# Optimization experiments

Measured on AMD Instinct MI355X. Metric: run time of the kernel, lower is better.

Reference implementation:

```python
import jax, jax.numpy as jnp
import numpy as np

SEQ, B, H, OUT = 128, 256, 1024, 128


def _linear_params(key, out_dim, in_dim):
    kw, kb = jax.random.split(key)
    bound = 1.0 / np.sqrt(in_dim)
    W = jax.random.uniform(kw, (out_dim, in_dim), jnp.float32, -bound, bound)
    b = jax.random.uniform(kb, (out_dim,), jnp.float32, -bound, bound)
    return W, b


def setup_inputs() -> dict:
    key = jax.random.key(0)
    keys = jax.random.split(key, 10)
    x = jax.random.normal(keys[0], (SEQ, B), jnp.float32)
    Wfx, bfx = _linear_params(keys[1], H, 1)
    Wfh, bfh = _linear_params(keys[2], H, H)
    Wix, bix = _linear_params(keys[3], H, 1)
    Wih, bih = _linear_params(keys[4], H, H)
    Wgx, bgx = _linear_params(keys[5], H, 1)
    Wgh, bgh = _linear_params(keys[6], H, H)
    Wox, box = _linear_params(keys[7], H, 1)
    Woh, boh = _linear_params(keys[8], H, H)
    Wph, bph = _linear_params(keys[9], OUT, H)
    return dict(x=x, Wfx=Wfx, bfx=bfx, Wfh=Wfh, bfh=bfh,
                Wix=Wix, bix=bix, Wih=Wih, bih=bih,
                Wgx=Wgx, bgx=bgx, Wgh=Wgh, bgh=bgh,
                Wox=Wox, box=box, Woh=Woh, boh=boh,
                Wph=Wph, bph=bph)


def reference(x, Wfx, bfx, Wfh, bfh, Wix, bix, Wih, bih,
              Wgx, bgx, Wgh, bgh, Wox, box, Woh, boh, Wph, bph):
    # Fuse the 8 per-gate linears into two GEMMs per step (x-proj and h-proj),
    # gate order: f, i, g, o.
    Wx = jnp.concatenate([Wfx, Wix, Wgx, Wox], axis=0)      # (4H, 1)
    bx = jnp.concatenate([bfx, bix, bgx, box], axis=0)       # (4H,)
    Wh = jnp.concatenate([Wfh, Wih, Wgh, Woh], axis=0)       # (4H, H)
    bh = jnp.concatenate([bfh, bih, bgh, boh], axis=0)       # (4H,)
    Hdim = Wfh.shape[0]
    Bsz = x.shape[1]

    # x projection has input_dim=1: precompute for all timesteps at once.
    zx_all = x[:, :, None] * Wx[:, 0][None, None, :] + bx     # (S, B, 4H)

    def step(carry, zx):
        h, c = carry
        z = zx + h @ Wh.T + bh                                # (B, 4H)
        f = jax.nn.sigmoid(z[:, 0 * Hdim:1 * Hdim])
        i = jax.nn.sigmoid(z[:, 1 * Hdim:2 * Hdim])
        g = jnp.tanh(z[:, 2 * Hdim:3 * Hdim])
        o = jax.nn.sigmoid(z[:, 3 * Hdim:4 * Hdim])
        c = g * i + c * f
        h = jnp.tanh(c) * o
        return (h, c), None

    h0 = jnp.zeros((Bsz, Hdim), x.dtype)
    c0 = jnp.zeros((Bsz, Hdim), x.dtype)
    (h, c), _ = jax.lax.scan(step, (h0, c0), zx_all)
    logits = h @ Wph.T + bph                                  # (B, OUT)
    return jax.nn.softmax(logits, axis=-1)
```

## Files before the change

kernel.cpp:

```cpp
#include <hip/hip_runtime.h>
#include <hip/hip_fp16.h>
#include <cstdint>
#include <cstddef>

#define SEQ   128
#define BATCH 256
#define HDIM  1024
#define ODIM  128
#define NBLK  256

typedef _Float16 half_t;
typedef _Float16 half8 __attribute__((ext_vector_type(8)));
typedef float    f32x4 __attribute__((ext_vector_type(4)));
typedef unsigned long long u64;

#define LDS_P_OFF    131072
#define LDS_HS_OFF   (LDS_P_OFF + 2 * 64 * 36 * 4)
#define LDS_BYTES    (LDS_HS_OFF + 64 * 16 * 2)

#define HBUF_BYTES   524288
#define FLAGS_OFF    ((size_t)129 * HBUF_BYTES)

__device__ __forceinline__ float sigmoidf_(float z) {
    return 1.0f / (1.0f + __expf(-z));
}
__device__ __forceinline__ float tanhf_(float z) {
    z = fminf(fmaxf(z, -30.0f), 30.0f);
    float e = __expf(2.0f * z);
    return (e - 1.0f) / (e + 1.0f);
}

__global__ __launch_bounds__(256) void lstm_init(int* __restrict__ flags) {
    flags[blockIdx.x * 256 + threadIdx.x] = 0;
}

__global__ __launch_bounds__(512, 2) void lstm_persist(
    const float* __restrict__ x,
    const float* __restrict__ Wfh, const float* __restrict__ Wih,
    const float* __restrict__ Wgh, const float* __restrict__ Woh,
    const float* __restrict__ Wfx, const float* __restrict__ Wix,
    const float* __restrict__ Wgx, const float* __restrict__ Wox,
    const float* __restrict__ bfx, const float* __restrict__ bix,
    const float* __restrict__ bgx, const float* __restrict__ box,
    const float* __restrict__ bfh, const float* __restrict__ bih,
    const float* __restrict__ bgh, const float* __restrict__ boh,
    const float* __restrict__ Wph, const float* __restrict__ bph,
    char* __restrict__ wsbase, float* __restrict__ out)
{
    extern __shared__ char smem[];
    half_t* Bs = (half_t*)smem;
    float*  P  = (float*)(smem + LDS_P_OFF);
    half_t* Hs = (half_t*)(smem + LDS_HS_OFF);
    int* flags = (int*)(wsbase + FLAGS_OFF);

    const int tid  = threadIdx.x;
    const int blk  = blockIdx.x;
    const int grp  = blk & 3;
    const int by   = blk >> 2;
    const int m0   = grp << 6;
    const int u0   = by << 4;

    const int w    = tid >> 6;
    const int lane = tid & 63;
    const int l15  = lane & 15;
    const int q    = lane >> 4;
    const int kh   = w >> 2;
    const int mh   = w & 3;

    {
        const float* Wh[4] = {Wfh, Wih, Wgh, Woh};
        for (int d = tid; d < 8192; d += 512) {
            const int ul = d & 15, qq = (d >> 4) & 3, g = (d >> 6) & 3;
            const int kk = (d >> 8) & 15, kh2 = d >> 12;
            const float* src = Wh[g] + (size_t)(u0 + ul) * HDIM
                             + kh2 * 512 + kk * 32 + qq * 8;
            const float4 v0 = *(const float4*)src;
            const float4 v1 = *(const float4*)(src + 4);
            half8 hv;
            hv[0] = (half_t)v0.x; hv[1] = (half_t)v0.y;
            hv[2] = (half_t)v0.z; hv[3] = (half_t)v0.w;
            hv[4] = (half_t)v1.x; hv[5] = (half_t)v1.y;
            hv[6] = (half_t)v1.z; hv[7] = (half_t)v1.w;
            *(half8*)(Bs + (size_t)d * 8) = hv;
        }
    }

    const int u = u0 + l15;
    const float bf = bfx[u] + bfh[u], bi = bix[u] + bih[u];
    const float bg = bgx[u] + bgh[u], bo = box[u] + boh[u];
    const float wf = Wfx[u], wi = Wix[u], wg = Wgx[u], wo = Wox[u];

    f32x4 creg = {0.f, 0.f, 0.f, 0.f};

    __syncthreads();

    for (int t = 0; t < SEQ; ++t) {
        const half_t* hin  = (const half_t*)(wsbase + (size_t)t * HBUF_BYTES);
        half_t*       hout = (half_t*)(wsbase + (size_t)(t + 1) * HBUF_BYTES);

        f32x4 acc[4] = {};

        if (t > 0) {
            const half_t* abase = hin + (size_t)(m0 + 16 * mh + l15) * HDIM
                                + kh * 512 + q * 8;
            half8 a[16];
#pragma unroll
            for (int kk = 0; kk < 16; ++kk)
                a[kk] = *(const half8*)(abase + kk * 32);
#pragma unroll
            for (int kk = 0; kk < 16; ++kk) {
                half8 bb[4];
#pragma unroll
                for (int g = 0; g < 4; ++g)
                    bb[g] = *(const half8*)(Bs +
                        ((size_t)((kh << 12) + (kk << 8) + (g << 6) + (q << 4) + l15)) * 8);
#pragma unroll
                for (int g = 0; g < 4; ++g)
                    acc[g] = __builtin_amdgcn_mfma_f32_16x16x32_f16(
                        a[kk], bb[g], acc[g], 0, 0, 0);
            }
        }

        if (kh == 1) {
#pragma unroll
            for (int g = 0; g < 4; ++g)
                *(f32x4*)&P[(size_t)((mh >> 1) * 64 + (g << 4) + l15) * 36
                            + (mh & 1) * 16 + (q << 2)] = acc[g];
        }
        __syncthreads();

        if (kh == 0) {
            const int lr0 = (mh << 4) + (q << 2);
            const float4 xv = *(const float4*)&x[t * BATCH + m0 + lr0];
            const int pb = ((mh >> 1) * 64 + l15) * 36 + (mh & 1) * 16 + (q << 2);
            f32x4 zf = acc[0] + *(const f32x4*)&P[pb];
            f32x4 zi = acc[1] + *(const f32x4*)&P[pb + 16 * 36];
            f32x4 zg = acc[2] + *(const f32x4*)&P[pb + 32 * 36];
            f32x4 zo = acc[3] + *(const f32x4*)&P[pb + 48 * 36];
#pragma unroll
            for (int e = 0; e < 4; ++e) {
                const float xe = (e == 0) ? xv.x : (e == 1) ? xv.y
                               : (e == 2) ? xv.z : xv.w;
                const float fg = sigmoidf_(zf[e] + xe * wf + bf);
                const float ig = sigmoidf_(zi[e] + xe * wi + bi);
                const float gg = tanhf_  (zg[e] + xe * wg + bg);
                const float og = sigmoidf_(zo[e] + xe * wo + bo);
                const float cn = gg * ig + creg[e] * fg;
                creg[e] = cn;
                Hs[(lr0 + e) * 16 + l15] = (half_t)(tanhf_(cn) * og);
            }
        }
        __syncthreads();

        if (tid < 256) {
            const int lr = tid >> 2, p = tid & 3;
            const u64 v = *(const u64*)&Hs[lr * 16 + p * 4];
            u64* dst = (u64*)(hout + (size_t)(m0 + lr) * HDIM + u0 + p * 4);
            __hip_atomic_store(dst, v, __ATOMIC_RELAXED, __HIP_MEMORY_SCOPE_AGENT);
        }
        asm volatile("s_waitcnt vmcnt(0)" ::: "memory");
        __syncthreads();

        if (tid == 0)
            __hip_atomic_store(&flags[(t << 8) + (grp << 6) + by], 1,
                               __ATOMIC_RELAXED, __HIP_MEMORY_SCOPE_AGENT);
        if (w == 0) {
            const int* pf = &flags[(t << 8) + (grp << 6)];
            for (;;) {
                const int v = __hip_atomic_load(&pf[lane], __ATOMIC_RELAXED,
                                                __HIP_MEMORY_SCOPE_AGENT);
                if (__all(v == 1)) break;
                __builtin_amdgcn_s_sleep(1);
            }
        }
        asm volatile("" ::: "memory");
        __syncthreads();
    }

    const int row = (grp << 6) + by;
    float* sm     = (float*)smem;
    float* hrow   = sm;
    float* psum   = sm + 1024;
    float* logits = sm + 1536;
    const half_t* hf = (const half_t*)(wsbase + (size_t)SEQ * HBUF_BYTES)
                     + ((size_t)row << 10);

    for (int k = tid; k < HDIM; k += 512) hrow[k] = (float)hf[k];
    __syncthreads();

    const int j = tid & 127, qt = tid >> 7;
    const float4* wp = (const float4*)(Wph + (size_t)j * HDIM + qt * 256);
    const float4* hp = (const float4*)(hrow + qt * 256);
    float s = 0.0f;
#pragma unroll 8
    for (int k4 = 0; k4 < 64; ++k4) {
        const float4 wv = wp[k4];
        const float4 hv = hp[k4];
        s += wv.x * hv.x + wv.y * hv.y + wv.z * hv.z + wv.w * hv.w;
    }
    psum[tid] = s;
    __syncthreads();
    if (tid < ODIM)
        logits[tid] = psum[tid] + psum[tid + 128] + psum[tid + 256]
                    + psum[tid + 384] + bph[tid];
    __syncthreads();
    if (tid < ODIM) {
        float mx = -1e30f;
        for (int i = 0; i < ODIM; ++i) mx = fmaxf(mx, logits[i]);
        psum[tid] = __expf(logits[tid] - mx);
    }
    __syncthreads();
    if (tid < ODIM) {
        float ssum = 0.0f;
        for (int i = 0; i < ODIM; ++i) ssum += psum[i];
        out[row * ODIM + tid] = psum[tid] / ssum;
    }
}

extern "C" void kernel_launch(void* const* d_in, const int* in_sizes, int n_in,
                              void* d_out, int out_size, void* d_ws, size_t ws_size,
                              hipStream_t stream) {
    const float* x   = (const float*)d_in[0];
    const float* Wfx = (const float*)d_in[1];
    const float* bfx = (const float*)d_in[2];
    const float* Wfh = (const float*)d_in[3];
    const float* bfh = (const float*)d_in[4];
    const float* Wix = (const float*)d_in[5];
    const float* bix = (const float*)d_in[6];
    const float* Wih = (const float*)d_in[7];
    const float* bih = (const float*)d_in[8];
    const float* Wgx = (const float*)d_in[9];
    const float* bgx = (const float*)d_in[10];
    const float* Wgh = (const float*)d_in[11];
    const float* bgh = (const float*)d_in[12];
    const float* Wox = (const float*)d_in[13];
    const float* box = (const float*)d_in[14];
    const float* Woh = (const float*)d_in[15];
    const float* boh = (const float*)d_in[16];
    const float* Wph = (const float*)d_in[17];
    const float* bph = (const float*)d_in[18];
    float* outp = (float*)d_out;

    char* ws = (char*)d_ws;
    int* flags = (int*)(ws + FLAGS_OFF);

    lstm_init<<<128, 256, 0, stream>>>(flags);

    (void)hipFuncSetAttribute((const void*)lstm_persist,
                              hipFuncAttributeMaxDynamicSharedMemorySize,
                              LDS_BYTES);

    void* args[] = {
        (void*)&x,
        (void*)&Wfh, (void*)&Wih, (void*)&Wgh, (void*)&Woh,
        (void*)&Wfx, (void*)&Wix, (void*)&Wgx, (void*)&Wox,
        (void*)&bfx, (void*)&bix, (void*)&bgx, (void*)&box,
        (void*)&bfh, (void*)&bih, (void*)&bgh, (void*)&boh,
        (void*)&Wph, (void*)&bph,
        (void*)&ws, (void*)&outp
    };
    (void)hipLaunchCooperativeKernel((const void*)lstm_persist,
                                     dim3(NBLK), dim3(512),
                                     args, LDS_BYTES, stream);
}
```

Measured before the change: 1.108 ms.

## Split each block's batch rows into two halves and overlap their recurrence steps

Each persistent block now handles two 32-row batch groups (A and B) instead of one 64-row group. Group B's MFMA work runs while group A's h writes and flag signalling are in flight, and the next step's A-operand loads are issued early after each group's barrier. Wave roles are also reassigned: one wave pair computes gates while the others spill partial sums to a padded LDS buffer, and flags shrink to 16-bit. This is meant to hide inter-block synchronisation latency behind compute, at the cost of more barriers, more registers for the two prefetched A tiles, and more complex flag ordering.

Result: slower. 1.974 ms (+78.1%).

```diff
diff --git a/kernel.cpp b/kernel.cpp
--- a/kernel.cpp
+++ b/kernel.cpp
@@ -13,10 +13,12 @@
 typedef _Float16 half8 __attribute__((ext_vector_type(8)));
 typedef float    f32x4 __attribute__((ext_vector_type(4)));
 typedef unsigned long long u64;
-
+typedef unsigned short flag_t;
+
+#define P_STRIDE     18
 #define LDS_P_OFF    131072
-#define LDS_HS_OFF   (LDS_P_OFF + 2 * 64 * 36 * 4)
-#define LDS_BYTES    (LDS_HS_OFF + 64 * 16 * 2)
+#define LDS_HS_OFF   (LDS_P_OFF + 192 * P_STRIDE * 4)
+#define LDS_BYTES    (LDS_HS_OFF + 32 * 16 * 2)
 
 #define HBUF_BYTES   524288
 #define FLAGS_OFF    ((size_t)129 * HBUF_BYTES)
@@ -51,13 +53,14 @@
     half_t* Bs = (half_t*)smem;
     float*  P  = (float*)(smem + LDS_P_OFF);
     half_t* Hs = (half_t*)(smem + LDS_HS_OFF);
-    int* flags = (int*)(wsbase + FLAGS_OFF);
+    flag_t* flags = (flag_t*)(wsbase + FLAGS_OFF);
 
     const int tid  = threadIdx.x;
     const int blk  = blockIdx.x;
-    const int grp  = blk & 3;
-    const int by   = blk >> 2;
-    const int m0   = grp << 6;
+    const int by   = blk & 63;
+    const int p    = blk >> 6;
+    const int rgA  = p << 1;
+    const int rgB  = rgA | 1;
     const int u0   = by << 4;
 
     const int w    = tid >> 6;
@@ -65,7 +68,9 @@
     const int l15  = lane & 15;
     const int q    = lane >> 4;
     const int kh   = w >> 2;
-    const int mh   = w & 3;
+    const int mh   = (w >> 1) & 1;
+    const int gh   = w & 1;
+    const bool gatew = (kh == 0) && (gh == 0);
 
     {
         const float* Wh[4] = {Wfh, Wih, Wgh, Woh};
@@ -90,94 +95,165 @@
     const float bg = bgx[u] + bgh[u], bo = box[u] + boh[u];
     const float wf = Wfx[u], wi = Wix[u], wg = Wgx[u], wo = Wox[u];
 
-    f32x4 creg = {0.f, 0.f, 0.f, 0.f};
+    f32x4 cregA = {0.f, 0.f, 0.f, 0.f};
+    f32x4 cregB = {0.f, 0.f, 0.f, 0.f};
+    half8 aA[16], aB[16];
 
     __syncthreads();
 
     for (int t = 0; t < SEQ; ++t) {
-        const half_t* hin  = (const half_t*)(wsbase + (size_t)t * HBUF_BYTES);
-        half_t*       hout = (half_t*)(wsbase + (size_t)(t + 1) * HBUF_BYTES);
-
-        f32x4 acc[4] = {};
-
+        half_t* hout = (half_t*)(wsbase + (size_t)(t + 1) * HBUF_BYTES);
+
+        f32x4 accA[2] = {};
         if (t > 0) {
-            const half_t* abase = hin + (size_t)(m0 + 16 * mh + l15) * HDIM
+#pragma unroll
+            for (int kk = 0; kk < 16; ++kk) {
+                const half8 b0 = *(const half8*)(Bs +
+                    ((size_t)((kh << 12) + (kk << 8) + ((2 * gh + 0) << 6) + (q << 4) + l15)) * 8);
+                const half8 b1 = *(const half8*)(Bs +
+                    ((size_t)((kh << 12) + (kk << 8) + ((2 * gh + 1) << 6) + (q << 4) + l15)) * 8);
+                accA[0] = __builtin_amdgcn_mfma_f32_16x16x32_f16(aA[kk], b0, accA[0], 0, 0, 0);
+                accA[1] = __builtin_amdgcn_mfma_f32_16x16x32_f16(aA[kk], b1, accA[1], 0, 0, 0);
+            }
+        }
+        if (!gatew) {
+            const int s = (kh << 1) + gh - 1;
+#pragma unroll
+            for (int j = 0; j < 2; ++j)
+                *(f32x4*)&P[(size_t)((((mh * 3 + s) << 1) + j) * 16 + l15) * P_STRIDE + (q << 2)]
+                    = accA[j];
+        }
+        __syncthreads();
+        if (gatew) {
+            const int lr0 = (mh << 4) + (q << 2);
+            const float4 xv = *(const float4*)&x[t * BATCH + rgA * 32 + lr0];
+            const int pq = q << 2;
+            f32x4 z0 = accA[0] + *(const f32x4*)&P[(size_t)((((mh * 3 + 1) << 1) + 0) * 16 + l15) * P_STRIDE + pq];
+            f32x4 z1 = accA[1] + *(const f32x4*)&P[(size_t)((((mh * 3 + 1) << 1) + 1) * 16 + l15) * P_STRIDE + pq];
+            f32x4 z2 = *(const f32x4*)&P[(size_t)((((mh * 3 + 0) << 1) + 0) * 16 + l15) * P_STRIDE + pq]
+                     + *(const f32x4*)&P[(size_t)((((mh * 3 + 2) << 1) + 0) * 16 + l15) * P_STRIDE + pq];
+            f32x4 z3 = *(const f32x4*)&P[(size_t)((((mh * 3 + 0) << 1) + 1) * 16 + l15) * P_STRIDE + pq]
+                     + *(const f32x4*)&P[(size_t)((((mh * 3 + 2) << 1) + 1) * 16 + l15) * P_STRIDE + pq];
+#pragma unroll
+            for (int e = 0; e < 4; ++e) {
+                const float xe = (e == 0) ? xv.x : (e == 1) ? xv.y : (e == 2) ? xv.z : xv.w;
+                const float fg = sigmoidf_(z0[e] + xe * wf + bf);
+                const float ig = sigmoidf_(z1[e] + xe * wi + bi);
+                const float gg = tanhf_  (z2[e] + xe * wg + bg);
+                const float og = sigmoidf_(z3[e] + xe * wo + bo);
+                const float cn = gg * ig + cregA[e] * fg;
+                cregA[e] = cn;
+                Hs[(lr0 + e) * 16 + l15] = (half_t)(tanhf_(cn) * og);
+            }
+        }
+        __syncthreads();
+        if (tid < 128) {
+            const int lr = tid >> 2, pc = tid & 3;
+            const u64 v = *(const u64*)&Hs[lr * 16 + pc * 4];
+            u64* dst = (u64*)(hout + (size_t)(rgA * 32 + lr) * HDIM + u0 + pc * 4);
+            __hip_atomic_store(dst, v, __ATOMIC_RELAXED, __HIP_MEMORY_SCOPE_AGENT);
+        }
+
+        f32x4 accB[2] = {};
+        if (t > 0) {
+#pragma unroll
+            for (int kk = 0; kk < 16; ++kk) {
+                const half8 b0 = *(const half8*)(Bs +
+                    ((size_t)((kh << 12) + (kk << 8) + ((2 * gh + 0) << 6) + (q << 4) + l15)) * 8);
+                const half8 b1 = *(const half8*)(Bs +
+                    ((size_t)((kh << 12) + (kk << 8) + ((2 * gh + 1) << 6) + (q << 4) + l15)) * 8);
+                accB[0] = __builtin_amdgcn_mfma_f32_16x16x32_f16(aB[kk], b0, accB[0], 0, 0, 0);
+                accB[1] = __builtin_amdgcn_mfma_f32_16x16x32_f16(aB[kk], b1, accB[1], 0, 0, 0);
+            }
+        }
+        asm volatile("s_waitcnt vmcnt(0)" ::: "memory");
+        if (tid == 0)
+            __hip_atomic_store(&flags[(size_t)(t * 8 + rgA) * 64 + by], (flag_t)1,
+                               __ATOMIC_RELAXED, __HIP_MEMORY_SCOPE_AGENT);
+
+        if (!gatew) {
+            const int s = (kh << 1) + gh - 1;
+#pragma unroll
+            for (int j = 0; j < 2; ++j)
+                *(f32x4*)&P[(size_t)((((mh * 3 + s) << 1) + j) * 16 + l15) * P_STRIDE + (q << 2)]
+                    = accB[j];
+        }
+        __syncthreads();
+        if (gatew) {
+            const int lr0 = (mh << 4) + (q << 2);
+            const float4 xv = *(const float4*)&x[t * BATCH + rgB * 32 + lr0];
+            const int pq = q << 2;
+            f32x4 z0 = accB[0] + *(const f32x4*)&P[(size_t)((((mh * 3 + 1) << 1) + 0) * 16 + l15) * P_STRIDE + pq];
+            f32x4 z1 = accB[1] + *(const f32x4*)&P[(size_t)((((mh * 3 + 1) << 1) + 1) * 16 + l15) * P_STRIDE + pq];
+            f32x4 z2 = *(const f32x4*)&P[(size_t)((((mh * 3 + 0) << 1) + 0) * 16 + l15) * P_STRIDE + pq]
+                     + *(const f32x4*)&P[(size_t)((((mh * 3 + 2) << 1) + 0) * 16 + l15) * P_STRIDE + pq];
+            f32x4 z3 = *(const f32x4*)&P[(size_t)((((mh * 3 + 0) << 1) + 1) * 16 + l15) * P_STRIDE + pq]
+                     + *(const f32x4*)&P[(size_t)((((mh * 3 + 2) << 1) + 1) * 16 + l15) * P_STRIDE + pq];
+#pragma unroll
+            for (int e = 0; e < 4; ++e) {
+                const float xe = (e == 0) ? xv.x : (e == 1) ? xv.y : (e == 2) ? xv.z : xv.w;
+                const float fg = sigmoidf_(z0[e] + xe * wf + bf);
+                const float ig = sigmoidf_(z1[e] + xe * wi + bi);
+                const float gg = tanhf_  (z2[e] + xe * wg + bg);
+                const float og = sigmoidf_(z3[e] + xe * wo + bo);
+                const float cn = gg * ig + cregB[e] * fg;
+                cregB[e] = cn;
+                Hs[(lr0 + e) * 16 + l15] = (half_t)(tanhf_(cn) * og);
+            }
+        }
+        __syncthreads();
+        if (tid < 128) {
+            const int lr = tid >> 2, pc = tid & 3;
+            const u64 v = *(const u64*)&Hs[lr * 16 + pc * 4];
+            u64* dst = (u64*)(hout + (size_t)(rgB * 32 + lr) * HDIM + u0 + pc * 4);
+            __hip_atomic_store(dst, v, __ATOMIC_RELAXED, __HIP_MEMORY_SCOPE_AGENT);
+        }
+
+        if (w == 0) {
+            const flag_t* pf = &flags[(size_t)(t * 8 + rgA) * 64];
+            for (;;) {
+                const flag_t v = __hip_atomic_load(&pf[lane], __ATOMIC_RELAXED,
+                                                   __HIP_MEMORY_SCOPE_AGENT);
+                if (__all(v == 1)) break;
+                __builtin_amdgcn_s_sleep(1);
+            }
+        }
+        asm volatile("" ::: "memory");
+        __syncthreads();
+        if (t < SEQ - 1) {
+            const half_t* abase = hout + (size_t)(rgA * 32 + mh * 16 + l15) * HDIM
                                 + kh * 512 + q * 8;
-            half8 a[16];
 #pragma unroll
             for (int kk = 0; kk < 16; ++kk)
-                a[kk] = *(const half8*)(abase + kk * 32);
-#pragma unroll
-            for (int kk = 0; kk < 16; ++kk) {
-                half8 bb[4];
-#pragma unroll
-                for (int g = 0; g < 4; ++g)
-                    bb[g] = *(const half8*)(Bs +
-                        ((size_t)((kh << 12) + (kk << 8) + (g << 6) + (q << 4) + l15)) * 8);
-#pragma unroll
-                for (int g = 0; g < 4; ++g)
-                    acc[g] = __builtin_amdgcn_mfma_f32_16x16x32_f16(
-                        a[kk], bb[g], acc[g], 0, 0, 0);
-            }
-        }
-
-        if (kh == 1) {
-#pragma unroll
-            for (int g = 0; g < 4; ++g)
-                *(f32x4*)&P[(size_t)((mh >> 1) * 64 + (g << 4) + l15) * 36
-                            + (mh & 1) * 16 + (q << 2)] = acc[g];
-        }
-        __syncthreads();
-
-        if (kh == 0) {
-            const int lr0 = (mh << 4) + (q << 2);
-            const float4 xv = *(const float4*)&x[t * BATCH + m0 + lr0];
-            const int pb = ((mh >> 1) * 64 + l15) * 36 + (mh & 1) * 16 + (q << 2);
-            f32x4 zf = acc[0] + *(const f32x4*)&P[pb];
-            f32x4 zi = acc[1] + *(const f32x4*)&P[pb + 16 * 36];
-            f32x4 zg = acc[2] + *(const f32x4*)&P[pb + 32 * 36];
-            f32x4 zo = acc[3] + *(const f32x4*)&P[pb + 48 * 36];
-#pragma unroll
-            for (int e = 0; e < 4; ++e) {
-                const float xe = (e == 0) ? xv.x : (e == 1) ? xv.y
-                               : (e == 2) ? xv.z : xv.w;
-                const float fg = sigmoidf_(zf[e] + xe * wf + bf);
-                const float ig = sigmoidf_(zi[e] + xe * wi + bi);
-                const float gg = tanhf_  (zg[e] + xe * wg + bg);
-                const float og = sigmoidf_(zo[e] + xe * wo + bo);
-                const float cn = gg * ig + creg[e] * fg;
-                creg[e] = cn;
-                Hs[(lr0 + e) * 16 + l15] = (half_t)(tanhf_(cn) * og);
-            }
-        }
-        __syncthreads();
-
-        if (tid < 256) {
-            const int lr = tid >> 2, p = tid & 3;
-            const u64 v = *(const u64*)&Hs[lr * 16 + p * 4];
-            u64* dst = (u64*)(hout + (size_t)(m0 + lr) * HDIM + u0 + p * 4);
-            __hip_atomic_store(dst, v, __ATOMIC_RELAXED, __HIP_MEMORY_SCOPE_AGENT);
-        }
-        asm volatile("s_waitcnt vmcnt(0)" ::: "memory");
-        __syncthreads();
-
+                aA[kk] = *(const half8*)(abase + kk * 32);
+            asm volatile("s_waitcnt vmcnt(16)" ::: "memory");
+        } else {
+            asm volatile("s_waitcnt vmcnt(0)" ::: "memory");
+        }
         if (tid == 0)
-            __hip_atomic_store(&flags[(t << 8) + (grp << 6) + by], 1,
+            __hip_atomic_store(&flags[(size_t)(t * 8 + rgB) * 64 + by], (flag_t)1,
                                __ATOMIC_RELAXED, __HIP_MEMORY_SCOPE_AGENT);
         if (w == 0) {
-            const int* pf = &flags[(t << 8) + (grp << 6)];
+            const flag_t* pf = &flags[(size_t)(t * 8 + rgB) * 64];
             for (;;) {
-                const int v = __hip_atomic_load(&pf[lane], __ATOMIC_RELAXED,
-                                                __HIP_MEMORY_SCOPE_AGENT);
+                const flag_t v = __hip_atomic_load(&pf[lane], __ATOMIC_RELAXED,
+                                                   __HIP_MEMORY_SCOPE_AGENT);
                 if (__all(v == 1)) break;
                 __builtin_amdgcn_s_sleep(1);
             }
         }
         asm volatile("" ::: "memory");
         __syncthreads();
-    }
-
-    const int row = (grp << 6) + by;
+        if (t < SEQ - 1) {
+            const half_t* abase = hout + (size_t)(rgB * 32 + mh * 16 + l15) * HDIM
+                                + kh * 512 + q * 8;
+#pragma unroll
+            for (int kk = 0; kk < 16; ++kk)
+                aB[kk] = *(const half8*)(abase + kk * 32);
+        }
+    }
+
+    const int row = blk;
     float* sm     = (float*)smem;
     float* hrow   = sm;
     float* psum   = sm + 1024;
```
